# Performance work log

Measured on AMD Instinct MI355X. Metric: run time of the kernel, lower is better.

Reference implementation:

```python
import jax, jax.numpy as jnp
import numpy as np
from jax import lax

TOP_N = 4
CAT_NUM = 4
IOU_THRESH = 0.25
PAD = 224
OUT_SZ = 224


def _gen_edge_anchors():
    # Faithful port of NTSNet._generate_default_anchor_maps for 448x448 input.
    settings = (
        dict(stride=32, size=48, scale=[2 ** (1.0 / 3.0), 2 ** (2.0 / 3.0)], ar=[0.667, 1, 1.5]),
        dict(stride=64, size=96, scale=[2 ** (1.0 / 3.0), 2 ** (2.0 / 3.0)], ar=[0.667, 1, 1.5]),
        dict(stride=128, size=192, scale=[1, 2 ** (1.0 / 3.0), 2 ** (2.0 / 3.0)], ar=[0.667, 1, 1.5]),
    )
    inp = np.array([448, 448], dtype=np.float32)
    edges = []
    for s in settings:
        stride = s['stride']
        oh, ow = np.ceil(inp / stride).astype(int)
        ostart = stride / 2.0
        oy = np.arange(ostart, ostart + stride * oh, stride, dtype=np.float32).reshape(oh, 1)
        ox = np.arange(ostart, ostart + stride * ow, stride, dtype=np.float32).reshape(1, ow)
        cy = np.broadcast_to(oy, (oh, ow)); cx = np.broadcast_to(ox, (oh, ow))
        for sc in s['scale']:
            for ar in s['ar']:
                h = s['size'] * sc / float(ar) ** 0.5
                w = s['size'] * sc * float(ar) ** 0.5
                e = np.stack([cy - h / 2.0, cx - w / 2.0, cy + h / 2.0, cx + w / 2.0], axis=-1).reshape(-1, 4)
                edges.append(e)
    return np.concatenate(edges, 0).astype(np.float32)

EDGE_ANCHORS = (_gen_edge_anchors() + PAD).astype(np.int32)  # [1614,4] (y0,x0,y1,x1) in padded coords
BOXES_F = jnp.asarray(EDGE_ANCHORS, jnp.float32)
BOXES_I = jnp.asarray(EDGE_ANCHORS, jnp.int32)
AREAS = (BOXES_F[:, 2] - BOXES_F[:, 0]) * (BOXES_F[:, 3] - BOXES_F[:, 1])
N_ANCHORS = EDGE_ANCHORS.shape[0]  # 1614


def _nms_single(scores):
    # Greedy hard NMS: pick top score, suppress IoU >= thresh, repeat TOP_N times.
    def step(valid, _):
        s = jnp.where(valid, scores, -jnp.inf)
        i = jnp.argmax(s)
        b = BOXES_F[i]
        sy = jnp.maximum(BOXES_F[:, 0], b[0]); sx = jnp.maximum(BOXES_F[:, 1], b[1])
        ey = jnp.minimum(BOXES_F[:, 2], b[2]); ex = jnp.minimum(BOXES_F[:, 3], b[3])
        ly = ey - sy; lx = ex - sx
        inter = jnp.where((ly < 0) | (lx < 0), 0.0, ly * lx)
        iou = inter / (AREAS + AREAS[i] - inter)
        return valid & (iou < IOU_THRESH), i
    _, idx = lax.scan(step, jnp.ones((N_ANCHORS,), bool), None, length=TOP_N)
    return idx  # [TOP_N] int


def _crop_resize(img, box):
    # img: [3, 896, 896]; box: int [4] = (y0,x0,y1,x1); bilinear, align_corners=True -> [3,224,224]
    hmax = img.shape[-1] - 1
    y0, x0, y1, x1 = box[0], box[1], box[2], box[3]
    t = jnp.arange(OUT_SZ, dtype=jnp.float32) / (OUT_SZ - 1.0)
    ys = y0.astype(jnp.float32) + t * (y1 - y0 - 1).astype(jnp.float32)
    xs = x0.astype(jnp.float32) + t * (x1 - x0 - 1).astype(jnp.float32)
    yf = jnp.floor(ys); xf = jnp.floor(xs)
    wy = (ys - yf)[None, :, None]; wx = (xs - xf)[None, None, :]
    yl = yf.astype(jnp.int32); yh = jnp.minimum(yl + 1, hmax)
    xl = xf.astype(jnp.int32); xh = jnp.minimum(xl + 1, hmax)
    g = lambda yi, xi: img[:, yi[:, None], xi[None, :]]
    top = g(yl, xl) * (1.0 - wx) + g(yl, xh) * wx
    bot = g(yh, xl) * (1.0 - wx) + g(yh, xh) * wx
    return top * (1.0 - wy) + bot * wy


def _conv(x, w, b, stride, pad):
    y = lax.conv_general_dilated(x, w, (stride, stride), ((pad, pad), (pad, pad)),
                                 dimension_numbers=('NCHW', 'OIHW', 'NCHW'))
    return y + b[None, :, None, None]


def _forward(x, bb_w, bb_b, w1, b1, t1w, t1b, w2, b2, t2w, t2b, w3, b3, t3w, t3b, cw, cb):
    B = x.shape[0]
    backbone = lambda z: jax.nn.relu(_conv(z, bb_w, bb_b, 32, 0))
    raw_pre = backbone(x)  # [B,2048,14,14]
    # Navigator unit
    y1 = jax.nn.relu(_conv(raw_pre, w1, b1, 1, 1))                                  # [B,128,14,14]
    z1 = (jnp.einsum('bchw,oc->bohw', y1, t1w) + t1b[None, :, None, None]).reshape(B, -1)
    y2 = jax.nn.relu(_conv(y1, w2, b2, 2, 1))                                        # [B,128,7,7]
    z2 = (jnp.einsum('bchw,oc->bohw', y2, t2w) + t2b[None, :, None, None]).reshape(B, -1)
    y3 = jax.nn.relu(_conv(y2, w3, b3, 2, 1))                                        # [B,128,4,4]
    z3 = (jnp.einsum('bchw,oc->bohw', y3, t3w) + t3b[None, :, None, None]).reshape(B, -1)
    rpn_score = jnp.concatenate([z1, z2, z3], axis=1)  # [B,1614]
    top_idx = jax.vmap(_nms_single)(rpn_score)          # [B,TOP_N]
    boxes = BOXES_I[top_idx]                            # [B,TOP_N,4]
    x_pad = jnp.pad(x, ((0, 0), (0, 0), (PAD, PAD), (PAD, PAD)))  # [B,3,896,896]
    parts = jax.vmap(lambda img, bs: jax.vmap(lambda b: _crop_resize(img, b))(bs))(x_pad, boxes)
    parts = lax.stop_gradient(parts).reshape(B * TOP_N, 3, OUT_SZ, OUT_SZ)  # .detach() in torch
    part_feat = backbone(parts).mean(axis=(2, 3)).reshape(B, TOP_N, 2048)
    part_feat = part_feat[:, :CAT_NUM].reshape(B, -1)   # [B,8192]
    raw_feat = lax.stop_gradient(raw_pre).mean(axis=(2, 3))  # [B,2048] (detached in torch)
    concat = jnp.concatenate([part_feat, raw_feat], axis=1)  # [B,10240]
    return concat @ cw.T + cb                           # [B,200]


def setup_inputs() -> dict:
    key = jax.random.key(0)
    ks = jax.random.split(key, 12)
    def w(k, shape, fan_in):
        return jax.random.normal(k, shape, jnp.float32) * np.float32(np.sqrt(2.0 / fan_in))
    return {
        'x': jax.random.normal(ks[0], (8, 3, 448, 448), jnp.float32),
        'bb_w': w(ks[1], (2048, 3, 32, 32), 3 * 32 * 32), 'bb_b': jnp.zeros((2048,), jnp.float32),
        'w1': w(ks[2], (128, 2048, 3, 3), 2048 * 9), 'b1': jnp.zeros((128,), jnp.float32),
        't1w': w(ks[3], (6, 128), 128), 't1b': jnp.zeros((6,), jnp.float32),
        'w2': w(ks[4], (128, 128, 3, 3), 128 * 9), 'b2': jnp.zeros((128,), jnp.float32),
        't2w': w(ks[5], (6, 128), 128), 't2b': jnp.zeros((6,), jnp.float32),
        'w3': w(ks[6], (128, 128, 3, 3), 128 * 9), 'b3': jnp.zeros((128,), jnp.float32),
        't3w': w(ks[7], (9, 128), 128), 't3b': jnp.zeros((9,), jnp.float32),
        'cw': w(ks[8], (200, 2048 * (CAT_NUM + 1)), 2048 * (CAT_NUM + 1)),
        'cb': jnp.zeros((200,), jnp.float32),
    }


def reference(x, bb_w, bb_b, w1, b1, t1w, t1b, w2, b2, t2w, t2b, w3, b3, t3w, t3b, cw, cb):
    return _forward(x, bb_w, bb_b, w1, b1, t1w, t1b, w2, b2, t2w, t2b, w3, b3, t3w, t3b, cw, cb)
```

## Files before the change

kernel.cpp:

```cpp
#include <hip/hip_runtime.h>
#include <math.h>


typedef _Float16 h8 __attribute__((ext_vector_type(8)));
typedef float f32x4 __attribute__((ext_vector_type(4)));

#define ASCALE 256.0f
#define WSCALE 16384.0f
#define RSCALE (1.0f / (256.0f * 16384.0f))

__device__ __forceinline__ void gload16(const void* g, void* l) {
  __builtin_amdgcn_global_load_lds(
      (__attribute__((address_space(1))) void*)(void*)(uintptr_t)g,
      (__attribute__((address_space(3))) void*)l, 16, 0, 0);
}

__global__ __launch_bounds__(256) void anchors_kernel(int* __restrict__ anch,
                                                      float* __restrict__ areas) {
  int i = blockIdx.x * 256 + threadIdx.x;
  if (i >= 1614) return;
  int stride, oh, a, pos;
  double size, sc;
  const double C13 = 1.2599210498948732;
  const double C23 = 1.5874010519681994;
  if (i < 1176) {
    stride = 32; size = 48.0; oh = 14; a = i / 196; pos = i % 196;
    sc = (a / 3 == 0) ? C13 : C23;
  } else if (i < 1470) {
    int r = i - 1176; stride = 64; size = 96.0; oh = 7; a = r / 49; pos = r % 49;
    sc = (a / 3 == 0) ? C13 : C23;
  } else {
    int r = i - 1470; stride = 128; size = 192.0; oh = 4; a = r / 16; pos = r % 16;
    int si = a / 3;
    sc = (si == 0) ? 1.0 : ((si == 1) ? C13 : C23);
  }
  int ari = a % 3;
  double ar = (ari == 0) ? 0.667 : ((ari == 1) ? 1.0 : 1.5);
  int gy = pos / oh, gx = pos % oh;
  float cy = 0.5f * (float)stride + (float)(stride * gy);
  float cx = 0.5f * (float)stride + (float)(stride * gx);
  double ss = sqrt(ar);
  double hd = (size * sc) / ss;
  double wd = (size * sc) * ss;
  float hh = (float)(hd * 0.5), wh = (float)(wd * 0.5);
  float e0 = (cy - hh) + 224.0f;
  float e1 = (cx - wh) + 224.0f;
  float e2 = (cy + hh) + 224.0f;
  float e3 = (cx + wh) + 224.0f;
  int y0 = (int)e0, x0 = (int)e1, y1i = (int)e2, x1i = (int)e3;
  anch[i * 4 + 0] = y0; anch[i * 4 + 1] = x0;
  anch[i * 4 + 2] = y1i; anch[i * 4 + 3] = x1i;
  areas[i] = (float)(y1i - y0) * (float)(x1i - x0);
}

__global__ __launch_bounds__(256) void permute_w(const float* __restrict__ w,
                                                 float* __restrict__ wp,
                                                 int Cout, int Cin) {
  int idx = blockIdx.x * 256 + threadIdx.x;
  int total = Cout * 9 * Cin;
  if (idx >= total) return;
  int c = idx % Cin; int t2 = idx / Cin; int tap = t2 % 9; int o = t2 / 9;
  wp[idx] = w[(o * Cin + c) * 9 + tap];
}

__global__ __launch_bounds__(256) void split_w(const float* __restrict__ src,
                                               _Float16* __restrict__ h,
                                               _Float16* __restrict__ l, int n8) {
  int i = blockIdx.x * 256 + threadIdx.x;
  if (i >= n8) return;
  float4 v0 = *(const float4*)(src + (size_t)i * 8);
  float4 v1 = *(const float4*)(src + (size_t)i * 8 + 4);
  float vv[8] = {v0.x, v0.y, v0.z, v0.w, v1.x, v1.y, v1.z, v1.w};
  h8 vh, vl;
#pragma unroll
  for (int j = 0; j < 8; ++j) {
    float s = vv[j] * WSCALE;
    _Float16 a = (_Float16)s;
    vh[j] = a; vl[j] = (_Float16)(s - (float)a);
  }
  *(h8*)(h + (size_t)i * 8) = vh;
  *(h8*)(l + (size_t)i * 8) = vl;
}

__global__ __launch_bounds__(256) void split_x(const float* __restrict__ x,
                                               _Float16* __restrict__ Ah,
                                               _Float16* __restrict__ Al) {
  int i = blockIdx.x * 256 + threadIdx.x;
  if (i >= 1664 * 384) return;
  int kq = i % 384, m = i / 384;
  int k = kq * 8;
  h8 vh = {}, vl = {};
  if (m < 1568) {
    int b = m / 196, pos = m % 196;
    int c = k >> 10, r = (k >> 5) & 31, col = k & 31;
    int py = (pos / 14) * 32 + r, px = (pos % 14) * 32 + col;
    const float* sp2 = x + (((size_t)(b * 3 + c) * 448 + py) * 448 + px);
    float4 v0 = *(const float4*)sp2;
    float4 v1 = *(const float4*)(sp2 + 4);
    float vv[8] = {v0.x, v0.y, v0.z, v0.w, v1.x, v1.y, v1.z, v1.w};
#pragma unroll
    for (int j = 0; j < 8; ++j) {
      float s = vv[j] * ASCALE;
      _Float16 a = (_Float16)s;
      vh[j] = a; vl[j] = (_Float16)(s - (float)a);
    }
  }
  *(h8*)(Ah + (size_t)m * 3072 + k) = vh;
  *(h8*)(Al + (size_t)m * 3072 + k) = vl;
}

__global__ __launch_bounds__(256) void gemm_bb_mfma(
    const _Float16* __restrict__ Ah, const _Float16* __restrict__ Al,
    const _Float16* __restrict__ Bh, const _Float16* __restrict__ Bl,
    float* __restrict__ P) {
  __shared__ __align__(16) char lds[65536];
  const int t = threadIdx.x;
  const int bid = blockIdx.x + 13 * blockIdx.y;
  const int orig = (bid & 7) * 26 + (bid >> 3);
  const int m0 = (orig % 13) * 128, n0 = (orig / 13) * 128;
  const int kz = blockIdx.z;
  const int lane = t & 63, w = t >> 6;
  const int wm = (w >> 1) * 64, wn = (w & 1) * 64;
  const int lrow = lane & 15, kg = lane >> 4;

  int offA[4], offB[4];
#pragma unroll
  for (int i = 0; i < 4; ++i) {
    int ba = (wm + i * 16 + lrow) * 64 + kg * 16;
    offA[i] = ba ^ (((ba >> 7) & 3) << 4);
    int bb2 = (wn + i * 16 + lrow) * 64 + kg * 16;
    offB[i] = bb2 ^ (((bb2 >> 7) & 3) << 4);
  }
  size_t gAo[2], gBo[2];
  int ldso[2];
#pragma unroll
  for (int e = 0; e < 2; ++e) {
    int p = e * 256 + t;
    int lsl = p ^ ((p >> 3) & 3);
    int row = lsl >> 2, kq = lsl & 3;
    gAo[e] = (size_t)(m0 + row) * 3072 + kq * 8;
    gBo[e] = (size_t)(n0 + row) * 3072 + kq * 8;
    ldso[e] = e * 4096 + (t & 192) * 16;
  }

  auto STAGE = [&](int buf, int k0) {
    char* L = lds + buf * 32768;
#pragma unroll
    for (int e = 0; e < 2; ++e) {
      gload16(Ah + gAo[e] + k0, L + ldso[e]);
      gload16(Al + gAo[e] + k0, L + 8192 + ldso[e]);
      gload16(Bh + gBo[e] + k0, L + 16384 + ldso[e]);
      gload16(Bl + gBo[e] + k0, L + 24576 + ldso[e]);
    }
  };

  f32x4 acc[4][4] = {};
  const int kbeg = kz * 1536, kend = kbeg + 1536;
  STAGE(0, kbeg);
  __syncthreads();
  int cur = 0;
  for (int k0 = kbeg; k0 < kend; k0 += 32) {
    if (k0 + 32 < kend) STAGE(cur ^ 1, k0 + 32);
    const char* L = lds + cur * 32768;
    h8 fah[4], fal[4], fbh[4], fbl[4];
#pragma unroll
    for (int i = 0; i < 4; ++i) {
      fah[i] = *(const h8*)(L + offA[i]);
      fal[i] = *(const h8*)(L + 8192 + offA[i]);
      fbh[i] = *(const h8*)(L + 16384 + offB[i]);
      fbl[i] = *(const h8*)(L + 24576 + offB[i]);
    }
#pragma unroll
    for (int i = 0; i < 4; ++i)
#pragma unroll
      for (int j = 0; j < 4; ++j)
        acc[i][j] = __builtin_amdgcn_mfma_f32_16x16x32_f16(fah[i], fbh[j], acc[i][j], 0, 0, 0);
#pragma unroll
    for (int i = 0; i < 4; ++i)
#pragma unroll
      for (int j = 0; j < 4; ++j)
        acc[i][j] = __builtin_amdgcn_mfma_f32_16x16x32_f16(fah[i], fbl[j], acc[i][j], 0, 0, 0);
#pragma unroll
    for (int i = 0; i < 4; ++i)
#pragma unroll
      for (int j = 0; j < 4; ++j)
        acc[i][j] = __builtin_amdgcn_mfma_f32_16x16x32_f16(fal[i], fbh[j], acc[i][j], 0, 0, 0);
    __syncthreads();
    cur ^= 1;
  }
  float* Pz = P + (size_t)kz * 1664 * 2048;
  const int prow = (lane >> 4) * 4;
#pragma unroll
  for (int i = 0; i < 4; ++i) {
#pragma unroll
    for (int j = 0; j < 4; ++j) {
      int n = n0 + wn + j * 16 + lrow;
#pragma unroll
      for (int r = 0; r < 4; ++r) {
        int m = m0 + wm + i * 16 + prow + r;
        Pz[(size_t)m * 2048 + n] = acc[i][j][r];
      }
    }
  }
}

template <int WRITE_SPLIT>
__global__ __launch_bounds__(256) void bb_reduce(const float* __restrict__ P,
                                                 const float* __restrict__ bias,
                                                 float* __restrict__ raw,
                                                 _Float16* __restrict__ h,
                                                 _Float16* __restrict__ l) {
  int idx = blockIdx.x * 256 + threadIdx.x;
  int m = idx >> 8, col = (idx & 255) * 8;
  if (WRITE_SPLIT) {
    if (m >= 1664) return;
    if (m >= 1568) {
      h8 z = {};
      *(h8*)(h + (size_t)m * 2048 + col) = z;
      *(h8*)(l + (size_t)m * 2048 + col) = z;
      return;
    }
  } else {
    if (m >= 1568) return;
  }
  size_t o = (size_t)m * 2048 + col;
  const float* p0 = P + o;
  const float* p1 = P + (size_t)1664 * 2048 + o;
  float4 a0 = *(const float4*)(p0);
  float4 a1 = *(const float4*)(p0 + 4);
  float4 c0 = *(const float4*)(p1);
  float4 c1 = *(const float4*)(p1 + 4);
  float4 b0 = *(const float4*)(bias + col);
  float4 b1 = *(const float4*)(bias + col + 4);
  float v[8];
  v[0] = fmaxf(fmaf(a0.x + c0.x, RSCALE, b0.x), 0.f);
  v[1] = fmaxf(fmaf(a0.y + c0.y, RSCALE, b0.y), 0.f);
  v[2] = fmaxf(fmaf(a0.z + c0.z, RSCALE, b0.z), 0.f);
  v[3] = fmaxf(fmaf(a0.w + c0.w, RSCALE, b0.w), 0.f);
  v[4] = fmaxf(fmaf(a1.x + c1.x, RSCALE, b1.x), 0.f);
  v[5] = fmaxf(fmaf(a1.y + c1.y, RSCALE, b1.y), 0.f);
  v[6] = fmaxf(fmaf(a1.z + c1.z, RSCALE, b1.z), 0.f);
  v[7] = fmaxf(fmaf(a1.w + c1.w, RSCALE, b1.w), 0.f);
  *(float4*)(raw + o) = make_float4(v[0], v[1], v[2], v[3]);
  *(float4*)(raw + o + 4) = make_float4(v[4], v[5], v[6], v[7]);
  if (WRITE_SPLIT) {
    h8 vh, vl;
#pragma unroll
    for (int j = 0; j < 8; ++j) {
      float s = v[j] * ASCALE;
      _Float16 a = (_Float16)s;
      vh[j] = a; vl[j] = (_Float16)(s - (float)a);
    }
    *(h8*)(h + o) = vh;
    *(h8*)(l + o) = vl;
  }
}

__global__ __launch_bounds__(256) void gemm_nav_mfma(
    const _Float16* __restrict__ Ah, const _Float16* __restrict__ Al,
    const _Float16* __restrict__ Bh, const _Float16* __restrict__ Bl,
    float* __restrict__ part) {
  __shared__ __align__(16) char lds[65536];
  const int t = threadIdx.x;
  const int bid = blockIdx.x + 13 * blockIdx.y;
  const int orig = (bid & 7) * 52 + (bid >> 3);
  const int m0 = (orig % 13) * 128;
  const int sp = orig / 13;
  const int lane = t & 63, w = t >> 6;
  const int wm = (w >> 1) * 64, wn = (w & 1) * 64;
  const int lrow = lane & 15, kg = lane >> 4;

  int offA[4], offB[4];
#pragma unroll
  for (int i = 0; i < 4; ++i) {
    int ba = (wm + i * 16 + lrow) * 64 + kg * 16;
    offA[i] = ba ^ (((ba >> 7) & 3) << 4);
    int bb2 = (wn + i * 16 + lrow) * 64 + kg * 16;
    offB[i] = bb2 ^ (((bb2 >> 7) & 3) << 4);
  }
  size_t gBo[2];
  int ldso[2], akq8[2], ab[2], apy[2], apx[2], amv[2];
#pragma unroll
  for (int e = 0; e < 2; ++e) {
    int p = e * 256 + t;
    int lsl = p ^ ((p >> 3) & 3);
    int row = lsl >> 2, kq = lsl & 3;
    gBo[e] = (size_t)row * 18432 + kq * 8;
    ldso[e] = e * 4096 + (t & 192) * 16;
    int m = m0 + row;
    amv[e] = (m < 1568);
    int b = m / 196, pos = m % 196;
    ab[e] = b; apy[e] = pos / 14; apx[e] = pos % 14;
    akq8[e] = kq * 8;
  }

  auto STAGE = [&](int buf, int k0) {
    const int tap = k0 >> 11;
    const int c = k0 & 2047;
    const int dy = tap / 3 - 1, dx = tap % 3 - 1;
    char* L = lds + buf * 32768;
#pragma unroll
    for (int e = 0; e < 2; ++e) {
      int sy = apy[e] + dy, sx = apx[e] + dx;
      bool ok = amv[e] && ((unsigned)sy < 14u) && ((unsigned)sx < 14u);
      size_t rowi = ok ? (size_t)(ab[e] * 196 + sy * 14 + sx) : (size_t)1600;
      size_t ao = rowi * 2048 + c + akq8[e];
      gload16(Ah + ao, L + ldso[e]);
      gload16(Al + ao, L + 8192 + ldso[e]);
      gload16(Bh + gBo[e] + k0, L + 16384 + ldso[e]);
      gload16(Bl + gBo[e] + k0, L + 24576 + ldso[e]);
    }
  };

  f32x4 acc[4][4] = {};
  const int kbeg = sp * 576, kend = kbeg + 576;
  STAGE(0, kbeg);
  __syncthreads();
  int cur = 0;
  for (int k0 = kbeg; k0 < kend; k0 += 32) {
    if (k0 + 32 < kend) STAGE(cur ^ 1, k0 + 32);
    const char* L = lds + cur * 32768;
    h8 fah[4], fal[4], fbh[4], fbl[4];
#pragma unroll
    for (int i = 0; i < 4; ++i) {
      fah[i] = *(const h8*)(L + offA[i]);
      fal[i] = *(const h8*)(L + 8192 + offA[i]);
      fbh[i] = *(const h8*)(L + 16384 + offB[i]);
      fbl[i] = *(const h8*)(L + 24576 + offB[i]);
    }
#pragma unroll
    for (int i = 0; i < 4; ++i)
#pragma unroll
      for (int j = 0; j < 4; ++j)
        acc[i][j] = __builtin_amdgcn_mfma_f32_16x16x32_f16(fah[i], fbh[j], acc[i][j], 0, 0, 0);
#pragma unroll
    for (int i = 0; i < 4; ++i)
#pragma unroll
      for (int j = 0; j < 4; ++j)
        acc[i][j] = __builtin_amdgcn_mfma_f32_16x16x32_f16(fah[i], fbl[j], acc[i][j], 0, 0, 0);
#pragma unroll
    for (int i = 0; i < 4; ++i)
#pragma unroll
      for (int j = 0; j < 4; ++j)
        acc[i][j] = __builtin_amdgcn_mfma_f32_16x16x32_f16(fal[i], fbh[j], acc[i][j], 0, 0, 0);
    __syncthreads();
    cur ^= 1;
  }
  const int prow = (lane >> 4) * 4;
#pragma unroll
  for (int i = 0; i < 4; ++i) {
#pragma unroll
    for (int j = 0; j < 4; ++j) {
      int n = wn + j * 16 + lrow;
#pragma unroll
      for (int r = 0; r < 4; ++r) {
        int m = m0 + wm + i * 16 + prow + r;
        if (m < 1568)
          part[((size_t)sp * 1568 + m) * 128 + n] = acc[i][j][r] * RSCALE;
      }
    }
  }
}

__global__ __launch_bounds__(256) void y1_reduce(const float* __restrict__ part,
                                                 const float* __restrict__ b1,
                                                 float* __restrict__ y1) {
  int idx = blockIdx.x * 256 + threadIdx.x;
  if (idx >= 1568 * 128) return;
  int o = idx & 127;
  float s = b1[o];
#pragma unroll
  for (int sp = 0; sp < 32; ++sp) s += part[(size_t)sp * 1568 * 128 + idx];
  y1[idx] = fmaxf(s, 0.f);
}

__global__ __launch_bounds__(256) void conv3x3s2(const float* __restrict__ in,
                                                 const float* __restrict__ wp,
                                                 const float* __restrict__ bias,
                                                 float* __restrict__ out,
                                                 int Hin, int Hout) {
  int idx = blockIdx.x * 256 + threadIdx.x;
  int total = 8 * Hout * Hout * 128;
  if (idx >= total) return;
  int o = idx & 127; int pos = idx >> 7;
  int ox = pos % Hout; int t2 = pos / Hout; int oy = t2 % Hout; int b = t2 / Hout;
  float acc = bias[o];
  for (int dy = 0; dy < 3; ++dy) {
    int iy = 2 * oy - 1 + dy;
    if (iy < 0 || iy >= Hin) continue;
    for (int dx = 0; dx < 3; ++dx) {
      int ix = 2 * ox - 1 + dx;
      if (ix < 0 || ix >= Hin) continue;
      const float* ip = in + ((b * Hin + iy) * Hin + ix) * 128;
      const float* wgt = wp + (o * 9 + dy * 3 + dx) * 128;
#pragma unroll 4
      for (int c = 0; c < 128; c += 4) {
        float4 a = *(const float4*)(ip + c);
        float4 ww = *(const float4*)(wgt + c);
        acc += a.x * ww.x + a.y * ww.y + a.z * ww.z + a.w * ww.w;
      }
    }
  }
  out[idx] = fmaxf(acc, 0.f);
}

__global__ __launch_bounds__(256) void scores_kernel(
    const float* __restrict__ y1, const float* __restrict__ y2,
    const float* __restrict__ y3, const float* __restrict__ t1w,
    const float* __restrict__ t1b, const float* __restrict__ t2w,
    const float* __restrict__ t2b, const float* __restrict__ t3w,
    const float* __restrict__ t3b, float* __restrict__ scores) {
  int idx = blockIdx.x * 256 + threadIdx.x;
  if (idx >= 8 * 1614) return;
  int b = idx / 1614, sI = idx % 1614;
  const float* f; const float* w; float bias;
  if (sI < 1176) {
    int a = sI / 196;
    f = y1 + (b * 196 + (sI % 196)) * 128; w = t1w + a * 128; bias = t1b[a];
  } else if (sI < 1470) {
    int r = sI - 1176; int a = r / 49;
    f = y2 + (b * 49 + (r % 49)) * 128; w = t2w + a * 128; bias = t2b[a];
  } else {
    int r = sI - 1470; int a = r / 16;
    f = y3 + (b * 16 + (r % 16)) * 128; w = t3w + a * 128; bias = t3b[a];
  }
  float acc = 0.f;
  for (int c = 0; c < 128; c += 4) {
    float4 a4 = *(const float4*)(f + c);
    float4 w4 = *(const float4*)(w + c);
    acc += a4.x * w4.x + a4.y * w4.y + a4.z * w4.z + a4.w * w4.w;
  }
  scores[idx] = acc + bias;
}

__global__ __launch_bounds__(256) void nms_kernel(const float* __restrict__ scores,
                                                  const int* __restrict__ anch,
                                                  const float* __restrict__ areas,
                                                  int* __restrict__ boxes) {
  const int b = blockIdx.x, t = threadIdx.x;
  const float* s = scores + b * 1614;
  __shared__ unsigned char valid[1614];
  __shared__ float rv[256];
  __shared__ int ri[256];
  for (int i = t; i < 1614; i += 256) valid[i] = 1;
  __syncthreads();
  for (int n = 0; n < 4; ++n) {
    float best = -INFINITY; int bi = 0x7fffffff;
    for (int i = t; i < 1614; i += 256) {
      if (valid[i]) {
        float v = s[i];
        if (v > best || (v == best && i < bi)) { best = v; bi = i; }
      }
    }
    rv[t] = best; ri[t] = bi;
    __syncthreads();
    for (int off = 128; off > 0; off >>= 1) {
      if (t < off) {
        float ov = rv[t + off]; int oi = ri[t + off];
        if (ov > rv[t] || (ov == rv[t] && oi < ri[t])) { rv[t] = ov; ri[t] = oi; }
      }
      __syncthreads();
    }
    int sel = ri[0];
    if (sel > 1613) sel = 0;
    const int4 bb = ((const int4*)anch)[sel];
    const float Ai = areas[sel];
    if (t == 0) ((int4*)boxes)[b * 4 + n] = bb;
    __syncthreads();
    for (int i = t; i < 1614; i += 256) {
      if (!valid[i]) continue;
      const int4 ab = ((const int4*)anch)[i];
      float sy = fmaxf((float)ab.x, (float)bb.x);
      float sx = fmaxf((float)ab.y, (float)bb.y);
      float ey = fminf((float)ab.z, (float)bb.z);
      float ex = fminf((float)ab.w, (float)bb.w);
      float ly = ey - sy, lx = ex - sx;
      float inter = (ly < 0.f || lx < 0.f) ? 0.f : ly * lx;
      float iou = inter / (areas[i] + Ai - inter);
      if (iou >= 0.25f) valid[i] = 0;
    }
    __syncthreads();
  }
}

__global__ __launch_bounds__(256) void crop_kernel(const float* __restrict__ x,
                                                   const int* __restrict__ boxes,
                                                   _Float16* __restrict__ Ah,
                                                   _Float16* __restrict__ Al) {
  int idx = blockIdx.x * 256 + threadIdx.x;
  if (idx >= 32 * 3 * 224 * 224) return;
  int px = idx % 224; int t1 = idx / 224; int py = t1 % 224; int t2 = t1 / 224;
  int c = t2 % 3; int p = t2 / 3;
  int b = p >> 2;
  const int4 bb = ((const int4*)boxes)[p];
  float ty = (float)py / 223.0f;
  float txf = (float)px / 223.0f;
  float ys = (float)bb.x + ty * (float)(bb.z - bb.x - 1);
  float xs = (float)bb.y + txf * (float)(bb.w - bb.y - 1);
  float yf = floorf(ys), xf = floorf(xs);
  float wy = ys - yf, wx = xs - xf;
  int yl = (int)yf, xl = (int)xf;
  int yh = min(yl + 1, 895), xh = min(xl + 1, 895);
  const float* img = x + (size_t)(b * 3 + c) * 448 * 448;
  auto samp = [&](int yy, int xx) -> float {
    yy -= 224; xx -= 224;
    if (yy < 0 || yy >= 448 || xx < 0 || xx >= 448) return 0.f;
    return img[yy * 448 + xx];
  };
  float v00 = samp(yl, xl), v01 = samp(yl, xh);
  float v10 = samp(yh, xl), v11 = samp(yh, xh);
  float top = v00 * (1.f - wx) + v01 * wx;
  float bot = v10 * (1.f - wx) + v11 * wx;
  float val = top * (1.f - wy) + bot * wy;
  int i = py >> 5, r = py & 31, j = px >> 5, col = px & 31;
  int m = p * 49 + i * 7 + j;
  int k = (c << 10) + (r << 5) + col;
  float s = val * ASCALE;
  _Float16 a = (_Float16)s;
  Ah[(size_t)m * 3072 + k] = a;
  Al[(size_t)m * 3072 + k] = (_Float16)(s - (float)a);
}

__global__ __launch_bounds__(256) void mean_kernel(const float* __restrict__ in,
                                                   float* __restrict__ out,
                                                   int rows) {
  int g = blockIdx.x >> 3;
  int o = ((blockIdx.x & 7) << 8) + threadIdx.x;
  const float* base = in + ((size_t)g * rows) * 2048 + o;
  float s0 = 0.f, s1 = 0.f, s2 = 0.f, s3 = 0.f;
  int r = 0;
  for (; r + 4 <= rows; r += 4) {
    s0 += base[(size_t)(r + 0) * 2048];
    s1 += base[(size_t)(r + 1) * 2048];
    s2 += base[(size_t)(r + 2) * 2048];
    s3 += base[(size_t)(r + 3) * 2048];
  }
  for (; r < rows; ++r) s0 += base[(size_t)r * 2048];
  out[(size_t)g * 2048 + o] = ((s0 + s1) + (s2 + s3)) / (float)rows;
}

__global__ __launch_bounds__(256) void final_kernel(const float* __restrict__ pfeat,
                                                    const float* __restrict__ rfeat,
                                                    const float* __restrict__ cw,
                                                    const float* __restrict__ cb,
                                                    float* __restrict__ out) {
  int gw = (blockIdx.x * 256 + threadIdx.x) >> 6;
  int lane = threadIdx.x & 63;
  if (gw >= 1600) return;
  int b = gw / 200, j = gw % 200;
  const float* wr = cw + (size_t)j * 10240;
  const float* pf = pfeat + (size_t)b * 8192;
  float acc = 0.f;
  for (int k = lane * 4; k < 8192; k += 256) {
    float4 a = *(const float4*)(pf + k);
    float4 w = *(const float4*)(wr + k);
    acc += a.x * w.x + a.y * w.y + a.z * w.z + a.w * w.w;
  }
  const float* rf = rfeat + (size_t)b * 2048;
  const float* wr2 = wr + 8192;
  for (int k = lane * 4; k < 2048; k += 256) {
    float4 a = *(const float4*)(rf + k);
    float4 w = *(const float4*)(wr2 + k);
    acc += a.x * w.x + a.y * w.y + a.z * w.z + a.w * w.w;
  }
#pragma unroll
  for (int off = 32; off > 0; off >>= 1) acc += __shfl_down(acc, off, 64);
  if (lane == 0) out[b * 200 + j] = acc + cb[j];
}

extern "C" void kernel_launch(void* const* d_in, const int* in_sizes, int n_in,
                              void* d_out, int out_size, void* d_ws, size_t ws_size,
                              hipStream_t stream) {
  const float* x   = (const float*)d_in[0];
  const float* bbw = (const float*)d_in[1];
  const float* bbb = (const float*)d_in[2];
  const float* w1  = (const float*)d_in[3];
  const float* b1  = (const float*)d_in[4];
  const float* t1w = (const float*)d_in[5];
  const float* t1b = (const float*)d_in[6];
  const float* w2  = (const float*)d_in[7];
  const float* b2  = (const float*)d_in[8];
  const float* t2w = (const float*)d_in[9];
  const float* t2b = (const float*)d_in[10];
  const float* w3  = (const float*)d_in[11];
  const float* b3  = (const float*)d_in[12];
  const float* t3w = (const float*)d_in[13];
  const float* t3b = (const float*)d_in[14];
  const float* cw  = (const float*)d_in[15];
  const float* cb  = (const float*)d_in[16];
  float* out = (float*)d_out;

  char* p = (char*)d_ws;
  auto alloc = [&](size_t bytes) -> char* {
    char* r = p; p += (bytes + 255) & ~(size_t)255; return r;
  };
  int*      anch  = (int*)     alloc((size_t)1614 * 4 * 4);
  float*    areas = (float*)   alloc((size_t)1614 * 4);
  float*    w1p   = (float*)   alloc((size_t)128 * 18432 * 4);
  _Float16* bWh   = (_Float16*)alloc((size_t)2048 * 3072 * 2);
  _Float16* bWl   = (_Float16*)alloc((size_t)2048 * 3072 * 2);
  _Float16* w1h   = (_Float16*)alloc((size_t)128 * 18432 * 2);
  _Float16* w1l   = (_Float16*)alloc((size_t)128 * 18432 * 2);
  _Float16* Ahh   = (_Float16*)alloc((size_t)1664 * 3072 * 2);
  _Float16* All   = (_Float16*)alloc((size_t)1664 * 3072 * 2);
  _Float16* rawh  = (_Float16*)alloc((size_t)1664 * 2048 * 2);
  _Float16* rawl  = (_Float16*)alloc((size_t)1664 * 2048 * 2);
  float*    raw   = (float*)   alloc((size_t)1568 * 2048 * 4);
  float*    w2p   = (float*)   alloc((size_t)128 * 9 * 128 * 4);
  float*    w3p   = (float*)   alloc((size_t)128 * 9 * 128 * 4);
  char*     big   = alloc((size_t)2 * 1664 * 2048 * 4);
  float*    Pbuf  = (float*)big;
  float*    y1s   = (float*)big;
  float*    y1v   = (float*)   alloc((size_t)1568 * 128 * 4);
  float*    y2v   = (float*)   alloc((size_t)392 * 128 * 4);
  float*    y3v   = (float*)   alloc((size_t)128 * 128 * 4);
  float*    sc    = (float*)   alloc((size_t)8 * 1614 * 4);
  int*      boxes = (int*)     alloc((size_t)8 * 4 * 4 * 4);
  float*    pfeat = (float*)   alloc((size_t)32 * 2048 * 4);
  float*    rfeat = (float*)   alloc((size_t)8 * 2048 * 4);

  anchors_kernel<<<7, 256, 0, stream>>>(anch, areas);
  permute_w<<<(128 * 9 * 2048 + 255) / 256, 256, 0, stream>>>(w1, w1p, 128, 2048);
  permute_w<<<(128 * 9 * 128 + 255) / 256, 256, 0, stream>>>(w2, w2p, 128, 128);
  permute_w<<<(128 * 9 * 128 + 255) / 256, 256, 0, stream>>>(w3, w3p, 128, 128);
  split_w<<<(2048 * 3072 / 8 + 255) / 256, 256, 0, stream>>>(bbw, bWh, bWl, 2048 * 3072 / 8);
  split_w<<<(128 * 18432 / 8 + 255) / 256, 256, 0, stream>>>(w1p, w1h, w1l, 128 * 18432 / 8);
  split_x<<<(1664 * 384 + 255) / 256, 256, 0, stream>>>(x, Ahh, All);

  gemm_bb_mfma<<<dim3(13, 16, 2), 256, 0, stream>>>(Ahh, All, bWh, bWl, Pbuf);
  bb_reduce<1><<<1664, 256, 0, stream>>>(Pbuf, bbb, raw, rawh, rawl);
  gemm_nav_mfma<<<dim3(13, 32), 256, 0, stream>>>(rawh, rawl, w1h, w1l, y1s);
  y1_reduce<<<(1568 * 128 + 255) / 256, 256, 0, stream>>>(y1s, b1, y1v);
  mean_kernel<<<64, 256, 0, stream>>>(raw, rfeat, 196);
  conv3x3s2<<<(8 * 7 * 7 * 128 + 255) / 256, 256, 0, stream>>>(y1v, w2p, b2, y2v, 14, 7);
  conv3x3s2<<<(8 * 4 * 4 * 128 + 255) / 256, 256, 0, stream>>>(y2v, w3p, b3, y3v, 7, 4);
  scores_kernel<<<(8 * 1614 + 255) / 256, 256, 0, stream>>>(
      y1v, y2v, y3v, t1w, t1b, t2w, t2b, t3w, t3b, sc);
  nms_kernel<<<8, 256, 0, stream>>>(sc, anch, areas, boxes);
  crop_kernel<<<(32 * 3 * 224 * 224) / 256, 256, 0, stream>>>(x, boxes, Ahh, All);
  gemm_bb_mfma<<<dim3(13, 16, 2), 256, 0, stream>>>(Ahh, All, bWh, bWl, Pbuf);
  bb_reduce<0><<<1568, 256, 0, stream>>>(Pbuf, bbb, raw, rawh, rawl);
  mean_kernel<<<256, 256, 0, stream>>>(raw, pfeat, 49);
  final_kernel<<<400, 256, 0, stream>>>(pfeat, rfeat, cw, cb, out);
}
```

Measured before the change: 391.5 us.

## Raise backbone GEMM split-K to four, fuse prep kernels, widen mean reduction

The backbone GEMM's split-K factor goes from 2 to 4, so the grid has 832 blocks instead of 416 to fill the GPU better, and bb_reduce now sums four partial slabs. The w1 permute and split are fused into one kernel, and the anchors and small weight permutes are merged into a single launch. mean_kernel now uses many more blocks with a shared-memory reduction across row groups. The trade-off is twice as much partial-sum traffic written and read through global memory, plus a larger workspace.

```diff
diff --git a/kernel.cpp b/kernel.cpp
--- a/kernel.cpp
+++ b/kernel.cpp
@@ -8,6 +8,7 @@
 #define ASCALE 256.0f
 #define WSCALE 16384.0f
 #define RSCALE (1.0f / (256.0f * 16384.0f))
+#define PSLAB ((size_t)1664 * 2048)
 
 __device__ __forceinline__ void gload16(const void* g, void* l) {
   __builtin_amdgcn_global_load_lds(
@@ -15,9 +16,7 @@
       (__attribute__((address_space(3))) void*)l, 16, 0, 0);
 }
 
-__global__ __launch_bounds__(256) void anchors_kernel(int* __restrict__ anch,
-                                                      float* __restrict__ areas) {
-  int i = blockIdx.x * 256 + threadIdx.x;
+__device__ void anchors_body(int i, int* anch, float* areas) {
   if (i >= 1614) return;
   int stride, oh, a, pos;
   double size, sc;
@@ -43,24 +42,27 @@
   double hd = (size * sc) / ss;
   double wd = (size * sc) * ss;
   float hh = (float)(hd * 0.5), wh = (float)(wd * 0.5);
-  float e0 = (cy - hh) + 224.0f;
-  float e1 = (cx - wh) + 224.0f;
-  float e2 = (cy + hh) + 224.0f;
-  float e3 = (cx + wh) + 224.0f;
-  int y0 = (int)e0, x0 = (int)e1, y1i = (int)e2, x1i = (int)e3;
+  int y0 = (int)((cy - hh) + 224.0f), x0 = (int)((cx - wh) + 224.0f);
+  int y1i = (int)((cy + hh) + 224.0f), x1i = (int)((cx + wh) + 224.0f);
   anch[i * 4 + 0] = y0; anch[i * 4 + 1] = x0;
   anch[i * 4 + 2] = y1i; anch[i * 4 + 3] = x1i;
   areas[i] = (float)(y1i - y0) * (float)(x1i - x0);
 }
 
-__global__ __launch_bounds__(256) void permute_w(const float* __restrict__ w,
-                                                 float* __restrict__ wp,
-                                                 int Cout, int Cin) {
-  int idx = blockIdx.x * 256 + threadIdx.x;
-  int total = Cout * 9 * Cin;
-  if (idx >= total) return;
-  int c = idx % Cin; int t2 = idx / Cin; int tap = t2 % 9; int o = t2 / 9;
-  wp[idx] = w[(o * Cin + c) * 9 + tap];
+__global__ __launch_bounds__(256) void prep_small(int* __restrict__ anch,
+                                                  float* __restrict__ areas,
+                                                  const float* __restrict__ w2,
+                                                  float* __restrict__ w2p,
+                                                  const float* __restrict__ w3,
+                                                  float* __restrict__ w3p) {
+  int b = blockIdx.x, t = threadIdx.x;
+  if (b < 7) { anchors_body(b * 256 + t, anch, areas); return; }
+  const float* src; float* dst; int idx;
+  if (b < 7 + 576) { src = w2; dst = w2p; idx = (b - 7) * 256 + t; }
+  else             { src = w3; dst = w3p; idx = (b - 583) * 256 + t; }
+  if (idx >= 128 * 9 * 128) return;
+  int c = idx % 128; int r2 = idx / 128; int tap = r2 % 9; int o = r2 / 9;
+  dst[idx] = src[(o * 128 + c) * 9 + tap];
 }
 
 __global__ __launch_bounds__(256) void split_w(const float* __restrict__ src,
@@ -80,6 +82,17 @@
   }
   *(h8*)(h + (size_t)i * 8) = vh;
   *(h8*)(l + (size_t)i * 8) = vl;
+}
+
+__global__ __launch_bounds__(256) void split_w1(const float* __restrict__ w1,
+                                                _Float16* __restrict__ h,
+                                                _Float16* __restrict__ l) {
+  int idx = blockIdx.x * 256 + threadIdx.x;
+  if (idx >= 128 * 9 * 2048) return;
+  int c = idx & 2047; int rest = idx >> 11; int tap = rest % 9; int o = rest / 9;
+  float v = w1[(o * 2048 + c) * 9 + tap] * WSCALE;
+  _Float16 a = (_Float16)v;
+  h[idx] = a; l[idx] = (_Float16)(v - (float)a);
 }
 
 __global__ __launch_bounds__(256) void split_x(const float* __restrict__ x,
@@ -155,7 +168,7 @@
   };
 
   f32x4 acc[4][4] = {};
-  const int kbeg = kz * 1536, kend = kbeg + 1536;
+  const int kbeg = kz * 768, kend = kbeg + 768;
   STAGE(0, kbeg);
   __syncthreads();
   int cur = 0;
@@ -188,7 +201,7 @@
     __syncthreads();
     cur ^= 1;
   }
-  float* Pz = P + (size_t)kz * 1664 * 2048;
+  float* Pz = P + (size_t)kz * PSLAB;
   const int prow = (lane >> 4) * 4;
 #pragma unroll
   for (int i = 0; i < 4; ++i) {
@@ -224,23 +237,19 @@
     if (m >= 1568) return;
   }
   size_t o = (size_t)m * 2048 + col;
-  const float* p0 = P + o;
-  const float* p1 = P + (size_t)1664 * 2048 + o;
-  float4 a0 = *(const float4*)(p0);
-  float4 a1 = *(const float4*)(p0 + 4);
-  float4 c0 = *(const float4*)(p1);
-  float4 c1 = *(const float4*)(p1 + 4);
-  float4 b0 = *(const float4*)(bias + col);
-  float4 b1 = *(const float4*)(bias + col + 4);
   float v[8];
-  v[0] = fmaxf(fmaf(a0.x + c0.x, RSCALE, b0.x), 0.f);
-  v[1] = fmaxf(fmaf(a0.y + c0.y, RSCALE, b0.y), 0.f);
-  v[2] = fmaxf(fmaf(a0.z + c0.z, RSCALE, b0.z), 0.f);
-  v[3] = fmaxf(fmaf(a0.w + c0.w, RSCALE, b0.w), 0.f);
-  v[4] = fmaxf(fmaf(a1.x + c1.x, RSCALE, b1.x), 0.f);
-  v[5] = fmaxf(fmaf(a1.y + c1.y, RSCALE, b1.y), 0.f);
-  v[6] = fmaxf(fmaf(a1.z + c1.z, RSCALE, b1.z), 0.f);
-  v[7] = fmaxf(fmaf(a1.w + c1.w, RSCALE, b1.w), 0.f);
+#pragma unroll
+  for (int q = 0; q < 2; ++q) {
+    float4 s0 = *(const float4*)(P + o + q * 4);
+    float4 s1 = *(const float4*)(P + PSLAB + o + q * 4);
+    float4 s2 = *(const float4*)(P + 2 * PSLAB + o + q * 4);
+    float4 s3 = *(const float4*)(P + 3 * PSLAB + o + q * 4);
+    float4 b = *(const float4*)(bias + col + q * 4);
+    v[q * 4 + 0] = fmaxf(fmaf((s0.x + s1.x) + (s2.x + s3.x), RSCALE, b.x), 0.f);
+    v[q * 4 + 1] = fmaxf(fmaf((s0.y + s1.y) + (s2.y + s3.y), RSCALE, b.y), 0.f);
+    v[q * 4 + 2] = fmaxf(fmaf((s0.z + s1.z) + (s2.z + s3.z), RSCALE, b.z), 0.f);
+    v[q * 4 + 3] = fmaxf(fmaf((s0.w + s1.w) + (s2.w + s3.w), RSCALE, b.w), 0.f);
+  }
   *(float4*)(raw + o) = make_float4(v[0], v[1], v[2], v[3]);
   *(float4*)(raw + o + 4) = make_float4(v[4], v[5], v[6], v[7]);
   if (WRITE_SPLIT) {
@@ -524,19 +533,19 @@
 __global__ __launch_bounds__(256) void mean_kernel(const float* __restrict__ in,
                                                    float* __restrict__ out,
                                                    int rows) {
-  int g = blockIdx.x >> 3;
-  int o = ((blockIdx.x & 7) << 8) + threadIdx.x;
-  const float* base = in + ((size_t)g * rows) * 2048 + o;
-  float s0 = 0.f, s1 = 0.f, s2 = 0.f, s3 = 0.f;
-  int r = 0;
-  for (; r + 4 <= rows; r += 4) {
-    s0 += base[(size_t)(r + 0) * 2048];
-    s1 += base[(size_t)(r + 1) * 2048];
-    s2 += base[(size_t)(r + 2) * 2048];
-    s3 += base[(size_t)(r + 3) * 2048];
-  }
-  for (; r < rows; ++r) s0 += base[(size_t)r * 2048];
-  out[(size_t)g * 2048 + o] = ((s0 + s1) + (s2 + s3)) / (float)rows;
+  int g = blockIdx.x >> 5, chunk = blockIdx.x & 31;
+  int col = chunk * 64 + (threadIdx.x & 63), rl = threadIdx.x >> 6;
+  const float* base = in + ((size_t)g * rows) * 2048 + col;
+  float s = 0.f;
+  for (int r = rl; r < rows; r += 4) s += base[(size_t)r * 2048];
+  __shared__ float red[4][64];
+  red[rl][threadIdx.x & 63] = s;
+  __syncthreads();
+  if (rl == 0) {
+    int c = threadIdx.x & 63;
+    out[(size_t)g * 2048 + col] =
+        ((red[0][c] + red[1][c]) + (red[2][c] + red[3][c])) / (float)rows;
+  }
 }
 
 __global__ __launch_bounds__(256) void final_kernel(const float* __restrict__ pfeat,
@@ -596,7 +605,6 @@
   };
   int*      anch  = (int*)     alloc((size_t)1614 * 4 * 4);
   float*    areas = (float*)   alloc((size_t)1614 * 4);
-  float*    w1p   = (float*)   alloc((size_t)128 * 18432 * 4);
   _Float16* bWh   = (_Float16*)alloc((size_t)2048 * 3072 * 2);
   _Float16* bWl   = (_Float16*)alloc((size_t)2048 * 3072 * 2);
   _Float16* w1h   = (_Float16*)alloc((size_t)128 * 18432 * 2);
@@ -608,7 +616,7 @@
   float*    raw   = (float*)   alloc((size_t)1568 * 2048 * 4);
   float*    w2p   = (float*)   alloc((size_t)128 * 9 * 128 * 4);
   float*    w3p   = (float*)   alloc((size_t)128 * 9 * 128 * 4);
-  char*     big   = alloc((size_t)2 * 1664 * 2048 * 4);
+  char*     big   = alloc((size_t)4 * PSLAB * 4);
   float*    Pbuf  = (float*)big;
   float*    y1s   = (float*)big;
   float*    y1v   = (float*)   alloc((size_t)1568 * 128 * 4);
@@ -619,27 +627,24 @@
   float*    pfeat = (float*)   alloc((size_t)32 * 2048 * 4);
   float*    rfeat = (float*)   alloc((size_t)8 * 2048 * 4);
 
-  anchors_kernel<<<7, 256, 0, stream>>>(anch, areas);
-  permute_w<<<(128 * 9 * 2048 + 255) / 256, 256, 0, stream>>>(w1, w1p, 128, 2048);
-  permute_w<<<(128 * 9 * 128 + 255) / 256, 256, 0, stream>>>(w2, w2p, 128, 128);
-  permute_w<<<(128 * 9 * 128 + 255) / 256, 256, 0, stream>>>(w3, w3p, 128, 128);
+  prep_small<<<7 + 576 + 576, 256, 0, stream>>>(anch, areas, w2, w2p, w3, w3p);
   split_w<<<(2048 * 3072 / 8 + 255) / 256, 256, 0, stream>>>(bbw, bWh, bWl, 2048 * 3072 / 8);
-  split_w<<<(128 * 18432 / 8 + 255) / 256, 256, 0, stream>>>(w1p, w1h, w1l, 128 * 18432 / 8);
+  split_w1<<<(128 * 9 * 2048 + 255) / 256, 256, 0, stream>>>(w1, w1h, w1l);
   split_x<<<(1664 * 384 + 255) / 256, 256, 0, stream>>>(x, Ahh, All);
 
-  gemm_bb_mfma<<<dim3(13, 16, 2), 256, 0, stream>>>(Ahh, All, bWh, bWl, Pbuf);
+  gemm_bb_mfma<<<dim3(13, 16, 4), 256, 0, stream>>>(Ahh, All, bWh, bWl, Pbuf);
   bb_reduce<1><<<1664, 256, 0, stream>>>(Pbuf, bbb, raw, rawh, rawl);
   gemm_nav_mfma<<<dim3(13, 32), 256, 0, stream>>>(rawh, rawl, w1h, w1l, y1s);
   y1_reduce<<<(1568 * 128 + 255) / 256, 256, 0, stream>>>(y1s, b1, y1v);
-  mean_kernel<<<64, 256, 0, stream>>>(raw, rfeat, 196);
+  mean_kernel<<<8 * 32, 256, 0, stream>>>(raw, rfeat, 196);
   conv3x3s2<<<(8 * 7 * 7 * 128 + 255) / 256, 256, 0, stream>>>(y1v, w2p, b2, y2v, 14, 7);
   conv3x3s2<<<(8 * 4 * 4 * 128 + 255) / 256, 256, 0, stream>>>(y2v, w3p, b3, y3v, 7, 4);
   scores_kernel<<<(8 * 1614 + 255) / 256, 256, 0, stream>>>(
       y1v, y2v, y3v, t1w, t1b, t2w, t2b, t3w, t3b, sc);
   nms_kernel<<<8, 256, 0, stream>>>(sc, anch, areas, boxes);
   crop_kernel<<<(32 * 3 * 224 * 224) / 256, 256, 0, stream>>>(x, boxes, Ahh, All);
-  gemm_bb_mfma<<<dim3(13, 16, 2), 256, 0, stream>>>(Ahh, All, bWh, bWl, Pbuf);
+  gemm_bb_mfma<<<dim3(13, 16, 4), 256, 0, stream>>>(Ahh, All, bWh, bWl, Pbuf);
   bb_reduce<0><<<1568, 256, 0, stream>>>(Pbuf, bbb, raw, rawh, rawl);
-  mean_kernel<<<256, 256, 0, stream>>>(raw, pfeat, 49);
+  mean_kernel<<<32 * 32, 256, 0, stream>>>(raw, pfeat, 49);
   final_kernel<<<400, 256, 0, stream>>>(pfeat, rfeat, cw, cb, out);
 }
```

Result: no change. 392.3 us (+0.2%).
